# Kernel tuning notes

Measured on AMD Instinct MI355X. Metric: run time of the kernel, lower is better.

## Reference

```python
import jax, jax.numpy as jnp
import numpy as np
import heapq

V = 10000   # vocab size (number of Huffman leaves)
H = 768     # hidden_size
B = 8       # batch
S = 256     # sen_len


def _build_tree():
    """Replicates make_heap/merge_nodes/make_codes: returns padded path tables.
    path_nodes[v, d] = internal-node index (0..V-2) at step d on v's code path,
    path_bits[v, d]  = branch taken (0=left, 1=right), path_mask = valid steps.
    """
    rng = np.random.default_rng(0)
    freqs = rng.integers(1, 1000, size=V)
    heap = [(int(freqs[i]), i, i) for i in range(V)]  # (freq, tiebreak, node_id)
    heapq.heapify(heap)
    left, right = {}, {}
    nid = V
    uid = V
    while len(heap) > 1:
        fa, _, a = heapq.heappop(heap)
        fb, _, b = heapq.heappop(heap)
        left[nid] = a
        right[nid] = b
        heapq.heappush(heap, (fa + fb, uid, nid))
        nid += 1
        uid += 1
    root = heap[0][2]
    paths = [None] * V
    stack = [(root, [], [])]
    while stack:
        n, pn, pb = stack.pop()
        if n < V:
            paths[n] = (pn, pb)
        else:
            idx = n - V  # internal node index into node_W/node_b
            stack.append((left[n], pn + [idx], pb + [0]))
            stack.append((right[n], pn + [idx], pb + [1]))
    D = max(len(p[0]) for p in paths)
    pn = np.zeros((V, D), np.int32)
    pb = np.zeros((V, D), np.int32)
    pm = np.zeros((V, D), bool)
    for i, (ns, bs) in enumerate(paths):
        L = len(ns)
        pn[i, :L] = ns
        pb[i, :L] = bs
        pm[i, :L] = True
    return pn, pb, pm


def setup_inputs() -> dict:
    key = jax.random.key(0)
    k1, k2, k3, k4 = jax.random.split(key, 4)
    pn, pb, pm = _build_tree()
    bound = float(1.0 / np.sqrt(H))  # torch nn.Linear default init
    return {
        "hidden": jax.random.normal(k1, (B, S, H), jnp.float32),
        "target": jax.random.randint(k2, (B, S), 0, V),
        "node_W": jax.random.uniform(k3, (V - 1, H, 2), jnp.float32, -bound, bound),
        "node_b": jax.random.uniform(k4, (V - 1, 2), jnp.float32, -bound, bound),
        "path_nodes": jnp.asarray(pn),
        "path_bits": jnp.asarray(pb),
        "path_mask": jnp.asarray(pm),
    }


def reference(hidden, target, node_W, node_b, path_nodes, path_bits, path_mask):
    # hidden: [B,S,H] -> [T,H]; target: [B,S] -> [T]
    h = hidden.reshape(-1, hidden.shape[-1])
    t = target.reshape(-1)
    nodes = path_nodes[t]          # [T, D] internal-node ids along each token's path
    bits = path_bits[t]            # [T, D] branch targets
    mask = path_mask[t]            # [T, D] valid-step mask
    Wg = node_W[nodes]             # [T, D, H, 2] gathered per-path linear weights
    bg = node_b[nodes]             # [T, D, 2]
    logits = jnp.einsum('th,tdho->tdo', h, Wg) + bg  # [T, D, 2]
    # Faithful to original: CrossEntropyLoss applied to Softmax OUTPUT (double softmax)
    probs = jax.nn.softmax(logits, axis=-1)
    logp = jax.nn.log_softmax(probs, axis=-1)
    ce = -jnp.take_along_axis(logp, bits[..., None], axis=-1)[..., 0]  # [T, D]
    # Original accumulates per-step CE (each over batch of 1) by summation
    return jnp.sum(jnp.where(mask, ce, jnp.zeros_like(ce)))
```

## Files before the change

kernel.cpp:

```cpp
#include <hip/hip_runtime.h>

#define HID 768
#define NTHREADS 256
#define WPB 4
#define MAXD_UNROLL 24

__global__ __launch_bounds__(NTHREADS) void huffman_tok_kernel(
    const float* __restrict__ hidden,
    const int*   __restrict__ target,
    const float* __restrict__ node_W,
    const float* __restrict__ node_b,
    const int*   __restrict__ path_nodes,
    const int*   __restrict__ path_bits,
    const void*  __restrict__ path_mask,
    float*       __restrict__ out,
    int D)
{
    const int t    = blockIdx.x;
    const int wave = threadIdx.x >> 6;
    const int lane = threadIdx.x & 63;

    const float2* __restrict__ h2 = (const float2*)(hidden + (long)t * HID);
    float2 hreg[HID / 2 / 64];
    #pragma unroll
    for (int j = 0; j < HID / 2 / 64; ++j) hreg[j] = h2[j * 64 + lane];

    const bool mask_is_byte = (*(const unsigned int*)path_mask) > 1u;
    const unsigned char* __restrict__ pm8  = (const unsigned char*)path_mask;
    const int*           __restrict__ pm32 = (const int*)path_mask;

    const int v = target[t];
    const long prow = (long)v * D;

    float lsum = 0.0f;

    auto do_step = [&](int d) {
        bool valid = (d < D);
        if (valid) valid = mask_is_byte ? (pm8[prow + d] != 0)
                                        : (pm32[prow + d] != 0);
        const long pidx = valid ? (prow + d) : prow;
        const int  n    = valid ? path_nodes[pidx] : 0;

        const float4* __restrict__ w4 =
            (const float4*)(node_W + (long)n * (HID * 2));

        float acc0 = 0.0f, acc1 = 0.0f;
        #pragma unroll
        for (int j = 0; j < HID / 2 / 64; ++j) {
            const float4 w = w4[j * 64 + lane];
            const float2 h = hreg[j];
            acc0 += h.x * w.x + h.y * w.z;
            acc1 += h.x * w.y + h.y * w.w;
        }
        #pragma unroll
        for (int off = 32; off > 0; off >>= 1) {
            acc0 += __shfl_xor(acc0, off, 64);
            acc1 += __shfl_xor(acc1, off, 64);
        }
        const float l0 = acc0 + node_b[n * 2 + 0];
        const float l1 = acc1 + node_b[n * 2 + 1];
        const float m  = fmaxf(l0, l1);
        const float e0 = __expf(l0 - m);
        const float e1 = __expf(l1 - m);
        const float s  = e0 + e1;
        const float p0 = e0 / s;
        const float p1 = e1 / s;
        const float lse = __logf(__expf(p0) + __expf(p1));
        const float pb  = path_bits[pidx] ? p1 : p0;
        lsum += valid ? (lse - pb) : 0.0f;
    };

    #pragma unroll
    for (int s = 0; s < MAXD_UNROLL / WPB; ++s)
        do_step(s * WPB + wave);
    for (int d = MAXD_UNROLL + wave; d < D; d += WPB)
        do_step(d);

    __shared__ float wsum[WPB];
    if (lane == 0) wsum[wave] = lsum;
    __syncthreads();
    if (threadIdx.x == 0) {
        float tot = 0.0f;
        #pragma unroll
        for (int w = 0; w < WPB; ++w) tot += wsum[w];
        atomicAdd(out, tot);
    }
}

extern "C" void kernel_launch(void* const* d_in, const int* in_sizes, int n_in,
                              void* d_out, int out_size, void* d_ws, size_t ws_size,
                              hipStream_t stream) {
    const float* hidden     = (const float*)d_in[0];
    const int*   target     = (const int*)d_in[1];
    const float* node_W     = (const float*)d_in[2];
    const float* node_b     = (const float*)d_in[3];
    const int*   path_nodes = (const int*)d_in[4];
    const int*   path_bits  = (const int*)d_in[5];
    const void*  path_mask  = (const void*)d_in[6];
    float* out = (float*)d_out;

    const int T   = in_sizes[0] / HID;
    const int Vm1 = in_sizes[3] / 2;
    const int V   = Vm1 + 1;
    const int D   = in_sizes[4] / V;

    hipMemsetAsync(d_out, 0, sizeof(float), stream);

    huffman_tok_kernel<<<dim3(T), dim3(NTHREADS), 0, stream>>>(
        hidden, target, node_W, node_b, path_nodes, path_bits, path_mask,
        out, D);
}
```

Measured before the change: 134.8 us.

## Split each wave into four 16-lane groups, one path step per group

```diff
diff --git a/kernel.cpp b/kernel.cpp
--- a/kernel.cpp
+++ b/kernel.cpp
@@ -3,9 +3,9 @@
 #define HID 768
 #define NTHREADS 256
 #define WPB 4
-#define MAXD_UNROLL 24
+#define NPJ (HID / 2 / 16)
 
-__global__ __launch_bounds__(NTHREADS) void huffman_tok_kernel(
+__global__ __launch_bounds__(NTHREADS) void huffman_g16_kernel(
     const float* __restrict__ hidden,
     const int*   __restrict__ target,
     const float* __restrict__ node_W,
@@ -17,27 +17,36 @@
     int D)
 {
     const int t    = blockIdx.x;
-    const int wave = threadIdx.x >> 6;
-    const int lane = threadIdx.x & 63;
+    const int tid  = threadIdx.x;
+    const int wave = tid >> 6;
+    const int lane = tid & 63;
+    const int g    = lane >> 4;
+    const int m    = lane & 15;
 
     const float2* __restrict__ h2 = (const float2*)(hidden + (long)t * HID);
-    float2 hreg[HID / 2 / 64];
+    float2 hreg[NPJ];
     #pragma unroll
-    for (int j = 0; j < HID / 2 / 64; ++j) hreg[j] = h2[j * 64 + lane];
+    for (int j = 0; j < NPJ; ++j) hreg[j] = h2[j * 16 + m];
 
     const bool mask_is_byte = (*(const unsigned int*)path_mask) > 1u;
     const unsigned char* __restrict__ pm8  = (const unsigned char*)path_mask;
     const int*           __restrict__ pm32 = (const int*)path_mask;
 
-    const int v = target[t];
+    const int  v    = target[t];
     const long prow = (long)v * D;
 
     float lsum = 0.0f;
+    const int rounds = (D + 15) >> 4;
 
-    auto do_step = [&](int d) {
+    for (int r = 0; r < rounds; ++r) {
+        const int d = r * 16 + wave * 4 + g;
+
         bool valid = (d < D);
         if (valid) valid = mask_is_byte ? (pm8[prow + d] != 0)
                                         : (pm32[prow + d] != 0);
+
+        if (__ballot(valid) == 0ull) continue;
+
         const long pidx = valid ? (prow + d) : prow;
         const int  n    = valid ? path_nodes[pidx] : 0;
 
@@ -46,40 +55,39 @@
 
         float acc0 = 0.0f, acc1 = 0.0f;
         #pragma unroll
-        for (int j = 0; j < HID / 2 / 64; ++j) {
-            const float4 w = w4[j * 64 + lane];
+        for (int j = 0; j < NPJ; ++j) {
+            const float4 w = w4[j * 16 + m];
             const float2 h = hreg[j];
             acc0 += h.x * w.x + h.y * w.z;
             acc1 += h.x * w.y + h.y * w.w;
         }
+
         #pragma unroll
-        for (int off = 32; off > 0; off >>= 1) {
+        for (int off = 8; off > 0; off >>= 1) {
             acc0 += __shfl_xor(acc0, off, 64);
             acc1 += __shfl_xor(acc1, off, 64);
         }
+
         const float l0 = acc0 + node_b[n * 2 + 0];
         const float l1 = acc1 + node_b[n * 2 + 1];
-        const float m  = fmaxf(l0, l1);
-        const float e0 = __expf(l0 - m);
-        const float e1 = __expf(l1 - m);
+        const float mx = fmaxf(l0, l1);
+        const float e0 = __expf(l0 - mx);
+        const float e1 = __expf(l1 - mx);
         const float s  = e0 + e1;
         const float p0 = e0 / s;
         const float p1 = e1 / s;
         const float lse = __logf(__expf(p0) + __expf(p1));
         const float pb  = path_bits[pidx] ? p1 : p0;
-        lsum += valid ? (lse - pb) : 0.0f;
-    };
+        lsum += (valid && m == 0) ? (lse - pb) : 0.0f;
+    }
 
     #pragma unroll
-    for (int s = 0; s < MAXD_UNROLL / WPB; ++s)
-        do_step(s * WPB + wave);
-    for (int d = MAXD_UNROLL + wave; d < D; d += WPB)
-        do_step(d);
+    for (int off = 32; off > 0; off >>= 1) lsum += __shfl_xor(lsum, off, 64);
 
     __shared__ float wsum[WPB];
     if (lane == 0) wsum[wave] = lsum;
     __syncthreads();
-    if (threadIdx.x == 0) {
+    if (tid == 0) {
         float tot = 0.0f;
         #pragma unroll
         for (int w = 0; w < WPB; ++w) tot += wsum[w];
@@ -106,7 +114,7 @@
 
     hipMemsetAsync(d_out, 0, sizeof(float), stream);
 
-    huffman_tok_kernel<<<dim3(T), dim3(NTHREADS), 0, stream>>>(
+    huffman_g16_kernel<<<dim3(T), dim3(NTHREADS), 0, stream>>>(
         hidden, target, node_W, node_b, path_nodes, path_bits, path_mask,
         out, D);
 }
```

Result: faster. 131.5 us (-2.4%).

## Precompute bf16 weight differences so each path step needs one dot product

Applied to the files above, without the earlier changes.

```diff
diff --git a/kernel.cpp b/kernel.cpp
--- a/kernel.cpp
+++ b/kernel.cpp
@@ -4,12 +4,45 @@
 #define NTHREADS 256
 #define WPB 4
 #define MAXD_UNROLL 24
+#define WD_OFF_BYTES (16u * 1024u * 1024u)
 
-__global__ __launch_bounds__(NTHREADS) void huffman_tok_kernel(
+__device__ __forceinline__ unsigned short f32_to_bf16(float x) {
+    unsigned u = __float_as_uint(x);
+    u += 0x7FFFu + ((u >> 16) & 1u);
+    return (unsigned short)(u >> 16);
+}
+__device__ __forceinline__ float bf16_to_f32(unsigned short u) {
+    return __uint_as_float(((unsigned)u) << 16);
+}
+
+__global__ __launch_bounds__(NTHREADS) void huffman_prep_kernel(
+    const float* __restrict__ node_W,
+    const float* __restrict__ node_b,
+    unsigned short* __restrict__ Wd,
+    float* __restrict__ bd,
+    int Vm1)
+{
+    const long idx    = (long)blockIdx.x * NTHREADS + threadIdx.x;
+    const long nquads = (long)Vm1 * (HID / 4);
+    if (idx < nquads) {
+        const float4* __restrict__ src = (const float4*)node_W + idx * 2;
+        const float4 a = src[0];
+        const float4 b = src[1];
+        ushort4 o;
+        o.x = f32_to_bf16(a.x - a.y);
+        o.y = f32_to_bf16(a.z - a.w);
+        o.z = f32_to_bf16(b.x - b.y);
+        o.w = f32_to_bf16(b.z - b.w);
+        ((ushort4*)Wd)[idx] = o;
+    }
+    if (idx < Vm1) bd[idx] = node_b[idx * 2] - node_b[idx * 2 + 1];
+}
+
+__global__ __launch_bounds__(NTHREADS) void huffman_gather_kernel(
     const float* __restrict__ hidden,
     const int*   __restrict__ target,
-    const float* __restrict__ node_W,
-    const float* __restrict__ node_b,
+    const unsigned short* __restrict__ Wd,
+    const float* __restrict__ bd,
     const int*   __restrict__ path_nodes,
     const int*   __restrict__ path_bits,
     const void*  __restrict__ path_mask,
@@ -20,16 +53,16 @@
     const int wave = threadIdx.x >> 6;
     const int lane = threadIdx.x & 63;
 
-    const float2* __restrict__ h2 = (const float2*)(hidden + (long)t * HID);
-    float2 hreg[HID / 2 / 64];
+    const float4* __restrict__ h4 = (const float4*)(hidden + (long)t * HID);
+    float4 hreg[3];
     #pragma unroll
-    for (int j = 0; j < HID / 2 / 64; ++j) hreg[j] = h2[j * 64 + lane];
+    for (int j = 0; j < 3; ++j) hreg[j] = h4[j * 64 + lane];
 
     const bool mask_is_byte = (*(const unsigned int*)path_mask) > 1u;
     const unsigned char* __restrict__ pm8  = (const unsigned char*)path_mask;
     const int*           __restrict__ pm32 = (const int*)path_mask;
 
-    const int v = target[t];
+    const int  v    = target[t];
     const long prow = (long)v * D;
 
     float lsum = 0.0f;
@@ -41,30 +74,25 @@
         const long pidx = valid ? (prow + d) : prow;
         const int  n    = valid ? path_nodes[pidx] : 0;
 
-        const float4* __restrict__ w4 =
-            (const float4*)(node_W + (long)n * (HID * 2));
+        const ushort4* __restrict__ w4 =
+            (const ushort4*)(Wd + (long)n * HID);
 
-        float acc0 = 0.0f, acc1 = 0.0f;
+        float acc = 0.0f;
         #pragma unroll
-        for (int j = 0; j < HID / 2 / 64; ++j) {
-            const float4 w = w4[j * 64 + lane];
-            const float2 h = hreg[j];
-            acc0 += h.x * w.x + h.y * w.z;
-            acc1 += h.x * w.y + h.y * w.w;
+        for (int j = 0; j < 3; ++j) {
+            const ushort4 w = w4[j * 64 + lane];
+            const float4  h = hreg[j];
+            acc += h.x * bf16_to_f32(w.x) + h.y * bf16_to_f32(w.y)
+                 + h.z * bf16_to_f32(w.z) + h.w * bf16_to_f32(w.w);
         }
+
         #pragma unroll
-        for (int off = 32; off > 0; off >>= 1) {
-            acc0 += __shfl_xor(acc0, off, 64);
-            acc1 += __shfl_xor(acc1, off, 64);
-        }
-        const float l0 = acc0 + node_b[n * 2 + 0];
-        const float l1 = acc1 + node_b[n * 2 + 1];
-        const float m  = fmaxf(l0, l1);
-        const float e0 = __expf(l0 - m);
-        const float e1 = __expf(l1 - m);
-        const float s  = e0 + e1;
-        const float p0 = e0 / s;
-        const float p1 = e1 / s;
+        for (int off = 32; off > 0; off >>= 1)
+            acc += __shfl_xor(acc, off, 64);
+
+        const float delta = acc + bd[n];
+        const float p0  = 1.0f / (1.0f + __expf(-delta));
+        const float p1  = 1.0f - p0;
         const float lse = __logf(__expf(p0) + __expf(p1));
         const float pb  = path_bits[pidx] ? p1 : p0;
         lsum += valid ? (lse - pb) : 0.0f;
@@ -104,9 +132,16 @@
     const int V   = Vm1 + 1;
     const int D   = in_sizes[4] / V;
 
+    unsigned short* Wd = (unsigned short*)d_ws;
+    float*          bd = (float*)((char*)d_ws + WD_OFF_BYTES);
+
     hipMemsetAsync(d_out, 0, sizeof(float), stream);
 
-    huffman_tok_kernel<<<dim3(T), dim3(NTHREADS), 0, stream>>>(
-        hidden, target, node_W, node_b, path_nodes, path_bits, path_mask,
-        out, D);
+    const long nquads = (long)Vm1 * (HID / 4);
+    const int  pblocks = (int)((nquads + NTHREADS - 1) / NTHREADS);
+    huffman_prep_kernel<<<dim3(pblocks), dim3(NTHREADS), 0, stream>>>(
+        node_W, node_b, Wd, bd, Vm1);
+
+    huffman_gather_kernel<<<dim3(T), dim3(NTHREADS), 0, stream>>>(
+        hidden, target, Wd, bd, path_nodes, path_bits, path_mask, out, D);
 }
```

Result: slower. 141.3 us (+4.9%).

## Split into path-packing pre-pass and one-wave-per-slot gather kernel

Applied to the files above, without the earlier changes.

```diff
diff --git a/kernel.cpp b/kernel.cpp
--- a/kernel.cpp
+++ b/kernel.cpp
@@ -3,87 +3,95 @@
 #define HID 768
 #define NTHREADS 256
 #define WPB 4
-#define MAXD_UNROLL 24
 
-__global__ __launch_bounds__(NTHREADS) void huffman_tok_kernel(
+__global__ __launch_bounds__(NTHREADS) void huffman_pack_kernel(
+    const int*  __restrict__ target,
+    const int*  __restrict__ path_nodes,
+    const int*  __restrict__ path_bits,
+    const void* __restrict__ path_mask,
+    int*        __restrict__ packed,
+    int T, int D)
+{
+    const int idx = blockIdx.x * NTHREADS + threadIdx.x;
+    if (idx >= T * D) return;
+    const int d = idx / T;
+    const int t = idx - d * T;
+
+    const bool mask_is_byte = (*(const unsigned int*)path_mask) > 1u;
+
+    const int  v  = target[t];
+    const long pr = (long)v * D + d;
+    const bool valid = mask_is_byte
+        ? (((const unsigned char*)path_mask)[pr] != 0)
+        : (((const int*)path_mask)[pr] != 0);
+
+    int p = 0;
+    if (valid) {
+        const int n = path_nodes[pr];
+        const int b = path_bits[pr];
+        p = (n << 2) | (b << 1) | 1;
+    }
+    packed[idx] = p;
+}
+
+__global__ __launch_bounds__(NTHREADS) void huffman_gather_kernel(
     const float* __restrict__ hidden,
-    const int*   __restrict__ target,
     const float* __restrict__ node_W,
     const float* __restrict__ node_b,
-    const int*   __restrict__ path_nodes,
-    const int*   __restrict__ path_bits,
-    const void*  __restrict__ path_mask,
+    const int*   __restrict__ packed,
     float*       __restrict__ out,
-    int D)
+    int T, int nslots)
 {
-    const int t    = blockIdx.x;
     const int wave = threadIdx.x >> 6;
     const int lane = threadIdx.x & 63;
-
-    const float2* __restrict__ h2 = (const float2*)(hidden + (long)t * HID);
-    float2 hreg[HID / 2 / 64];
-    #pragma unroll
-    for (int j = 0; j < HID / 2 / 64; ++j) hreg[j] = h2[j * 64 + lane];
-
-    const bool mask_is_byte = (*(const unsigned int*)path_mask) > 1u;
-    const unsigned char* __restrict__ pm8  = (const unsigned char*)path_mask;
-    const int*           __restrict__ pm32 = (const int*)path_mask;
-
-    const int v = target[t];
-    const long prow = (long)v * D;
+    const int slot = blockIdx.x * WPB + wave;
 
     float lsum = 0.0f;
 
-    auto do_step = [&](int d) {
-        bool valid = (d < D);
-        if (valid) valid = mask_is_byte ? (pm8[prow + d] != 0)
-                                        : (pm32[prow + d] != 0);
-        const long pidx = valid ? (prow + d) : prow;
-        const int  n    = valid ? path_nodes[pidx] : 0;
+    if (slot < nslots) {
+        const int p = packed[slot];
+        if (p & 1) {
+            const int d = slot / T;
+            const int t = slot - d * T;
+            const int n = p >> 2;
 
-        const float4* __restrict__ w4 =
-            (const float4*)(node_W + (long)n * (HID * 2));
+            const float4* __restrict__ w4 =
+                (const float4*)(node_W + (long)n * (HID * 2));
+            const float2* __restrict__ h2 =
+                (const float2*)(hidden + (long)t * HID);
 
-        float acc0 = 0.0f, acc1 = 0.0f;
-        #pragma unroll
-        for (int j = 0; j < HID / 2 / 64; ++j) {
-            const float4 w = w4[j * 64 + lane];
-            const float2 h = hreg[j];
-            acc0 += h.x * w.x + h.y * w.z;
-            acc1 += h.x * w.y + h.y * w.w;
+            float acc0 = 0.0f, acc1 = 0.0f;
+            #pragma unroll
+            for (int j = 0; j < HID / 2 / 64; ++j) {
+                const int q  = j * 64 + lane;
+                const float4 w = w4[q];
+                const float2 h = h2[q];
+                acc0 += h.x * w.x + h.y * w.z;
+                acc1 += h.x * w.y + h.y * w.w;
+            }
+
+            #pragma unroll
+            for (int off = 32; off > 0; off >>= 1) {
+                acc0 += __shfl_xor(acc0, off, 64);
+                acc1 += __shfl_xor(acc1, off, 64);
+            }
+
+            const float delta = (acc0 - acc1)
+                              + (node_b[n * 2 + 0] - node_b[n * 2 + 1]);
+            const float p0  = 1.0f / (1.0f + __expf(-delta));
+            const float p1  = 1.0f - p0;
+            const float lse = __logf(__expf(p0) + __expf(p1));
+            const float pb  = (p & 2) ? p1 : p0;
+            lsum = lse - pb;
         }
-        #pragma unroll
-        for (int off = 32; off > 0; off >>= 1) {
-            acc0 += __shfl_xor(acc0, off, 64);
-            acc1 += __shfl_xor(acc1, off, 64);
-        }
-        const float l0 = acc0 + node_b[n * 2 + 0];
-        const float l1 = acc1 + node_b[n * 2 + 1];
-        const float m  = fmaxf(l0, l1);
-        const float e0 = __expf(l0 - m);
-        const float e1 = __expf(l1 - m);
-        const float s  = e0 + e1;
-        const float p0 = e0 / s;
-        const float p1 = e1 / s;
-        const float lse = __logf(__expf(p0) + __expf(p1));
-        const float pb  = path_bits[pidx] ? p1 : p0;
-        lsum += valid ? (lse - pb) : 0.0f;
-    };
-
-    #pragma unroll
-    for (int s = 0; s < MAXD_UNROLL / WPB; ++s)
-        do_step(s * WPB + wave);
-    for (int d = MAXD_UNROLL + wave; d < D; d += WPB)
-        do_step(d);
+    }
 
     __shared__ float wsum[WPB];
     if (lane == 0) wsum[wave] = lsum;
     __syncthreads();
     if (threadIdx.x == 0) {
-        float tot = 0.0f;
-        #pragma unroll
-        for (int w = 0; w < WPB; ++w) tot += wsum[w];
-        atomicAdd(out, tot);
+        const float tot = (wsum[0] + wsum[1]) + (wsum[2] + wsum[3]);
+        if (tot != 0.0f) atomicAdd(out, tot);
     }
 }
 
@@ -104,9 +112,16 @@
     const int V   = Vm1 + 1;
     const int D   = in_sizes[4] / V;
 
+    int* packed = (int*)d_ws;
+    const int nslots = T * D;
+
     hipMemsetAsync(d_out, 0, sizeof(float), stream);
 
-    huffman_tok_kernel<<<dim3(T), dim3(NTHREADS), 0, stream>>>(
-        hidden, target, node_W, node_b, path_nodes, path_bits, path_mask,
-        out, D);
+    const int pblocks = (nslots + NTHREADS - 1) / NTHREADS;
+    huffman_pack_kernel<<<dim3(pblocks), dim3(NTHREADS), 0, stream>>>(
+        target, path_nodes, path_bits, path_mask, packed, T, D);
+
+    const int gblocks = (nslots + WPB - 1) / WPB;
+    huffman_gather_kernel<<<dim3(gblocks), dim3(NTHREADS), 0, stream>>>(
+        hidden, node_W, node_b, packed, out, T, nslots);
 }
```

After: 200.9 us. 1.49x slower.
